# Optimization experiments

Hardware: AMD Instinct MI355X
Metric: run time of the kernel (lower is better)

Reference implementation:

```python
import jax, jax.numpy as jnp
import numpy as np

HIDDEN = 2048
N_HEADS = 16
N_KV = 2
HEAD_DIM = HIDDEN // N_HEADS  # 128


def setup_inputs() -> dict:
    key = jax.random.key(0)
    ks = jax.random.split(key, 9)
    s = 0.02
    kv_dim = N_KV * HEAD_DIM
    return {
        "hidden_states": jax.random.normal(ks[0], (2, 2048, HIDDEN), jnp.float32),
        "Wq": jax.random.normal(ks[1], (HIDDEN, HIDDEN), jnp.float32) * s,
        "bq": jnp.zeros((HIDDEN,), jnp.float32),
        "Wk": jax.random.normal(ks[2], (HIDDEN, kv_dim), jnp.float32) * s,
        "bk": jnp.zeros((kv_dim,), jnp.float32),
        "Wv": jax.random.normal(ks[3], (HIDDEN, kv_dim), jnp.float32) * s,
        "bv": jnp.zeros((kv_dim,), jnp.float32),
        "Wo": jax.random.normal(ks[4], (HIDDEN, HIDDEN), jnp.float32) * s,
        "bo": jnp.zeros((HIDDEN,), jnp.float32),
    }


def reference(hidden_states, Wq, bq, Wk, bk, Wv, bv, Wo, bo):
    B, S, _ = hidden_states.shape
    scaling = HEAD_DIM ** (-0.5)
    rep = N_HEADS // N_KV

    q = hidden_states @ Wq + bq                      # [B,S,H*D]
    k = hidden_states @ Wk + bk                      # [B,S,KV*D]
    v = hidden_states @ Wv + bv

    q = q.reshape(B, S, N_HEADS, HEAD_DIM) * scaling
    k = k.reshape(B, S, N_KV, HEAD_DIM)
    v = v.reshape(B, S, N_KV, HEAD_DIM)
    # repeat_interleave KV heads to match query heads (faithful to source)
    k = jnp.repeat(k, rep, axis=2)                   # [B,S,H,D]
    v = jnp.repeat(v, rep, axis=2)

    attn = jnp.einsum('bqhd,bkhd->bhqk', q, k)       # [B,H,S,S] score matrix
    attn = jax.nn.softmax(attn, axis=-1)
    out = jnp.einsum('bhqk,bkhd->bqhd', attn, v)     # [B,S,H,D]
    out = out.reshape(B, S, N_HEADS * HEAD_DIM)
    return out @ Wo + bo
```

## Files before the change

kernel.cpp:

```cpp
#include <hip/hip_runtime.h>

typedef __bf16 bf16;
typedef __bf16 bf16x4 __attribute__((ext_vector_type(4)));
typedef __bf16 bf16x8 __attribute__((ext_vector_type(8)));
typedef float  f32x4  __attribute__((ext_vector_type(4)));

#define AS1 __attribute__((address_space(1)))
#define AS3 __attribute__((address_space(3)))

__device__ __forceinline__ void gload_lds16(const void* g, void* l) {
    __builtin_amdgcn_global_load_lds((const AS1 void*)g, (AS3 void*)l, 16, 0, 0);
}

__global__ __launch_bounds__(256) void prep(
    const float* __restrict__ X,  const float* __restrict__ Wq,
    const float* __restrict__ Wk, const float* __restrict__ Wv,
    const float* __restrict__ Wo, const float* __restrict__ bq,
    const float* __restrict__ bk, const float* __restrict__ bv,
    bf16* __restrict__ Xb, bf16* __restrict__ Wqkvt,
    bf16* __restrict__ Wot, float* __restrict__ bqkv)
{
    __shared__ float tile[32][33];
    int bid = blockIdx.x;
    if (bid < 8192) {
        int i = bid * 256 + threadIdx.x;
        float4 v = ((const float4*)X)[i];
        bf16x4 o = { (bf16)v.x, (bf16)v.y, (bf16)v.z, (bf16)v.w };
        ((bf16x4*)Xb)[i] = o;
        return;
    }
    bid -= 8192;
    const float* src; bf16* dst; int R, C, bx, by;
    if (bid < 4096)      { src = Wq; dst = Wqkvt;                      R = 2048; C = 2048; bx = bid & 63; by = bid >> 6; }
    else if (bid < 4608) { int t = bid - 4096; src = Wk; dst = Wqkvt + (size_t)2048 * 2048; R = 2048; C = 256; bx = t & 7; by = t >> 3; }
    else if (bid < 5120) { int t = bid - 4608; src = Wv; dst = Wqkvt + (size_t)2304 * 2048; R = 2048; C = 256; bx = t & 7; by = t >> 3; }
    else if (bid < 9216) { int t = bid - 5120; src = Wo; dst = Wot;    R = 2048; C = 2048; bx = t & 63; by = t >> 6; }
    else {
        int i = (bid - 9216) * 256 + threadIdx.x;
        if (i < 2048) bqkv[i] = bq[i];
        else if (i < 2304) bqkv[i] = bk[i - 2048];
        else if (i < 2560) bqkv[i] = bv[i - 2304];
        return;
    }
    int tx = threadIdx.x & 31, tg = threadIdx.x >> 5;
    int c0 = bx * 32, r0 = by * 32;
    #pragma unroll
    for (int j = tg; j < 32; j += 8)
        tile[j][tx] = src[(size_t)(r0 + j) * C + c0 + tx];
    __syncthreads();
    #pragma unroll
    for (int j = tg; j < 32; j += 8)
        dst[(size_t)(c0 + j) * R + r0 + tx] = (bf16)tile[tx][j];
}

__global__ __launch_bounds__(256) void transpose_v(
    const bf16* __restrict__ KV, bf16* __restrict__ VT)
{
    const int t = threadIdx.x;
    const int dg = t & 15;
    const int cg = (blockIdx.x << 4) | (t >> 4);
    const int kvh = blockIdx.y, b = blockIdx.z;
    const int tile = cg >> 3, cl = cg & 7;
    const int k0 = ((cl & 4) << 3) | ((cl & 3) << 2);

    const bf16* src = KV + ((size_t)(b * 2048 + tile * 64 + k0) * 512) + 256 + kvh * 128 + dg * 8;
    bf16x8 col[8];
    #pragma unroll
    for (int e = 0; e < 8; ++e) {
        int koff = ((e & 4) << 2) | (e & 3);
        col[e] = *(const bf16x8*)(src + (size_t)koff * 512);
    }
    bf16* dst = VT + ((size_t)((b * 2 + kvh) * 128 + dg * 8)) * 2048 + cg * 8;
    #pragma unroll
    for (int j = 0; j < 8; ++j) {
        bf16x8 row;
        #pragma unroll
        for (int e = 0; e < 8; ++e) row[e] = col[e][j];
        *(bf16x8*)(dst + (size_t)j * 2048) = row;
    }
}

template<int OUTBF>
__global__ __launch_bounds__(256) void gemm_bt(
    const bf16* __restrict__ A, const bf16* __restrict__ Bt,
    const float* __restrict__ bias, void* __restrict__ Cv,
    int M, int N, int K, float scale)
{
    __shared__ bf16 As[128 * 32];
    __shared__ bf16 Bs[128 * 32];
    const int tid = threadIdx.x;
    const int l = tid & 63, w = tid >> 6;
    const int wm = w >> 1, wn = w & 1;
    const size_t rowBase = (size_t)blockIdx.y * 128;
    const size_t colBase = (size_t)blockIdx.x * 128;

    f32x4 acc[4][4] = {};

    const int srow = l >> 2;
    const int schunk = (l & 3) ^ ((l >> 3) & 3);
    const int frow = l & 15;
    const int fswz = (frow >> 1) & 3;
    const int g = l >> 4;

    const bf16* Ag = A  + (rowBase + w * 32 + srow) * (size_t)K + schunk * 8;
    const bf16* Bg = Bt + (colBase + w * 32 + srow) * (size_t)K + schunk * 8;

    for (int k0 = 0; k0 < K; k0 += 32) {
        gload_lds16(Ag + k0,                  As + (w * 32) * 32);
        gload_lds16(Ag + 16 * (size_t)K + k0, As + (w * 32 + 16) * 32);
        gload_lds16(Bg + k0,                  Bs + (w * 32) * 32);
        gload_lds16(Bg + 16 * (size_t)K + k0, Bs + (w * 32 + 16) * 32);
        __syncthreads();

        bf16x8 af[4], bfr[4];
        #pragma unroll
        for (int mi = 0; mi < 4; ++mi)
            af[mi] = *(const bf16x8*)(As + (wm * 64 + mi * 16 + frow) * 32 + ((g ^ fswz) << 3));
        #pragma unroll
        for (int ni = 0; ni < 4; ++ni)
            bfr[ni] = *(const bf16x8*)(Bs + (wn * 64 + ni * 16 + frow) * 32 + ((g ^ fswz) << 3));
        #pragma unroll
        for (int mi = 0; mi < 4; ++mi)
            #pragma unroll
            for (int ni = 0; ni < 4; ++ni)
                acc[mi][ni] = __builtin_amdgcn_mfma_f32_16x16x32_bf16(af[mi], bfr[ni], acc[mi][ni], 0, 0, 0);
        __syncthreads();
    }

    const int cr = (l >> 4) * 4;
    const int cc = l & 15;
    #pragma unroll
    for (int ni = 0; ni < 4; ++ni) {
        const int col = (int)colBase + wn * 64 + ni * 16 + cc;
        const float bv = bias[col];
        #pragma unroll
        for (int mi = 0; mi < 4; ++mi) {
            #pragma unroll
            for (int r = 0; r < 4; ++r) {
                const size_t row = rowBase + wm * 64 + mi * 16 + cr + r;
                float v = (acc[mi][ni][r] + bv) * scale;
                if (OUTBF) ((bf16*)Cv)[row * N + col] = (bf16)v;
                else       ((float*)Cv)[row * N + col] = v;
            }
        }
    }
}

__global__ __launch_bounds__(256) void gemm_qkv(
    const bf16* __restrict__ A, const bf16* __restrict__ Bt,
    const float* __restrict__ bias, bf16* __restrict__ Qb, bf16* __restrict__ KVb,
    float qscale)
{
    constexpr int K = 2048;
    __shared__ bf16 As[128 * 32];
    __shared__ bf16 Bs[128 * 32];
    const int tid = threadIdx.x;
    const int l = tid & 63, w = tid >> 6;
    const int wm = w >> 1, wn = w & 1;
    const size_t rowBase = (size_t)blockIdx.y * 128;
    const size_t colBase = (size_t)blockIdx.x * 128;

    f32x4 acc[4][4] = {};

    const int srow = l >> 2;
    const int schunk = (l & 3) ^ ((l >> 3) & 3);
    const int frow = l & 15;
    const int fswz = (frow >> 1) & 3;
    const int g = l >> 4;

    const bf16* Ag = A  + (rowBase + w * 32 + srow) * (size_t)K + schunk * 8;
    const bf16* Bg = Bt + (colBase + w * 32 + srow) * (size_t)K + schunk * 8;

    for (int k0 = 0; k0 < K; k0 += 32) {
        gload_lds16(Ag + k0,                  As + (w * 32) * 32);
        gload_lds16(Ag + 16 * (size_t)K + k0, As + (w * 32 + 16) * 32);
        gload_lds16(Bg + k0,                  Bs + (w * 32) * 32);
        gload_lds16(Bg + 16 * (size_t)K + k0, Bs + (w * 32 + 16) * 32);
        __syncthreads();

        bf16x8 af[4], bfr[4];
        #pragma unroll
        for (int mi = 0; mi < 4; ++mi)
            af[mi] = *(const bf16x8*)(As + (wm * 64 + mi * 16 + frow) * 32 + ((g ^ fswz) << 3));
        #pragma unroll
        for (int ni = 0; ni < 4; ++ni)
            bfr[ni] = *(const bf16x8*)(Bs + (wn * 64 + ni * 16 + frow) * 32 + ((g ^ fswz) << 3));
        #pragma unroll
        for (int mi = 0; mi < 4; ++mi)
            #pragma unroll
            for (int ni = 0; ni < 4; ++ni)
                acc[mi][ni] = __builtin_amdgcn_mfma_f32_16x16x32_bf16(af[mi], bfr[ni], acc[mi][ni], 0, 0, 0);
        __syncthreads();
    }

    const bool isQ = colBase < 2048;
    bf16* Cb = isQ ? Qb : KVb;
    const int ldc = isQ ? 2048 : 512;
    const int coff = isQ ? 0 : 2048;
    const float s = isQ ? qscale : 1.0f;

    const int cr = (l >> 4) * 4;
    const int cc = l & 15;
    #pragma unroll
    for (int ni = 0; ni < 4; ++ni) {
        const int col = (int)colBase + wn * 64 + ni * 16 + cc;
        const float bv = bias[col];
        #pragma unroll
        for (int mi = 0; mi < 4; ++mi) {
            #pragma unroll
            for (int r = 0; r < 4; ++r) {
                const size_t row = rowBase + wm * 64 + mi * 16 + cr + r;
                Cb[row * ldc + (col - coff)] = (bf16)((acc[mi][ni][r] + bv) * s);
            }
        }
    }
}

__global__ __launch_bounds__(512, 4) void attn_fwd(
    const bf16* __restrict__ Q, const bf16* __restrict__ KV,
    const bf16* __restrict__ VT, bf16* __restrict__ O)
{
    constexpr int S = 2048;
    constexpr int LDKV = 512;
    constexpr int NT = S / 64;
    __shared__ bf16 Ks[2][64 * 128];
    __shared__ bf16 VTs[2][128 * 64];

    const int tid = threadIdx.x;
    const int l = tid & 63, w = tid >> 6;
    const int qt = blockIdx.x, h = blockIdx.y, b = blockIdx.z;
    const int kvh = h >> 3;
    const int lg = l >> 4, ll = l & 15;
    const int eh = (ll >> 2) & 1;

    bf16x8 qf[4];
    {
        const bf16* qp = Q + ((size_t)(b * S + qt * 128 + w * 16 + ll)) * 2048 + h * 128 + lg * 8;
        #pragma unroll
        for (int j = 0; j < 4; ++j) qf[j] = *(const bf16x8*)(qp + (j << 5));
    }

    const bf16* Kg  = KV + (size_t)b * S * LDKV + kvh * 128;
    const bf16* VTg = VT + ((size_t)(b * 2 + kvh) * 128) * S;

    const bf16* kg0 = Kg + (size_t)(w * 8 + lg) * LDKV + (ll ^ lg) * 8;
    const bf16* kg1 = Kg + (size_t)(w * 8 + 4 + lg) * LDKV + (ll ^ (4 + lg)) * 8;
    const bf16* vg0 = VTg + (size_t)(w * 16 + (l >> 3)) * S + (((l & 7) ^ ((l >> 3) & 7)) << 3);
    const bf16* vg1 = vg0 + 8 * (size_t)S;
    const int kd0 = (w * 8) * 128;
    const int kd1 = (w * 8 + 4) * 128;
    const int vd0 = w * 1024;
    const int vd1 = w * 1024 + 512;

    const int swz8 = (lg ^ (ll & 3)) << 3;
    const int kbE = ll * 128 + swz8 + eh * 32;
    const int kbO = ll * 128 + swz8 + (1 - eh) * 32;
    const int vbE = ll * 64 + swz8 + eh * 32;
    const int vbO = ll * 64 + swz8 + (1 - eh) * 32;

    bf16x8 vones;
    #pragma unroll
    for (int e = 0; e < 8; ++e) vones[e] = (bf16)1.0f;

    f32x4 of[8] = {};
    f32x4 of_l = {};

    gload_lds16(kg0, &Ks[0][kd0]);
    gload_lds16(kg1, &Ks[0][kd1]);
    gload_lds16(vg0, &VTs[0][vd0]);
    gload_lds16(vg1, &VTs[0][vd1]);
    __syncthreads();

    for (int t = 0; t < NT; ++t) {
        const int buf = t & 1;
        const bf16* kE = &Ks[buf][kbE];
        const bf16* kO = &Ks[buf][kbO];
        const bf16* vE = &VTs[buf][vbE];
        const bf16* vO = &VTs[buf][vbO];

        if (t + 1 < NT) {
            const size_t ko = (size_t)(t + 1) * 64 * LDKV;
            const int    vo = (t + 1) * 64;
            gload_lds16(kg0 + ko, &Ks[buf ^ 1][kd0]);
            gload_lds16(kg1 + ko, &Ks[buf ^ 1][kd1]);
            gload_lds16(vg0 + vo, &VTs[buf ^ 1][vd0]);
            gload_lds16(vg1 + vo, &VTs[buf ^ 1][vd1]);
        }

        f32x4 sc[4] = {};
        __builtin_amdgcn_s_setprio(1);
        #pragma unroll
        for (int ni = 0; ni < 4; ++ni) {
            bf16x8 k0f = *(const bf16x8*)(kE + ni * 2048);
            sc[ni] = __builtin_amdgcn_mfma_f32_16x16x32_bf16(k0f, qf[0], sc[ni], 0, 0, 0);
            bf16x8 k1f = *(const bf16x8*)(kO + ni * 2048);
            sc[ni] = __builtin_amdgcn_mfma_f32_16x16x32_bf16(k1f, qf[1], sc[ni], 0, 0, 0);
            bf16x8 k2f = *(const bf16x8*)(kE + ni * 2048 + 64);
            sc[ni] = __builtin_amdgcn_mfma_f32_16x16x32_bf16(k2f, qf[2], sc[ni], 0, 0, 0);
            bf16x8 k3f = *(const bf16x8*)(kO + ni * 2048 + 64);
            sc[ni] = __builtin_amdgcn_mfma_f32_16x16x32_bf16(k3f, qf[3], sc[ni], 0, 0, 0);
        }
        __builtin_amdgcn_s_setprio(0);

        float p[4][4];
        #pragma unroll
        for (int ni = 0; ni < 4; ++ni)
            #pragma unroll
            for (int r = 0; r < 4; ++r)
                p[ni][r] = __builtin_exp2f(sc[ni][r]);

        bf16x8 pa0, pa1;
        #pragma unroll
        for (int e = 0; e < 8; ++e) {
            pa0[e] = (bf16)p[(e >> 2)][e & 3];
            pa1[e] = (bf16)p[2 + (e >> 2)][e & 3];
        }

        __builtin_amdgcn_s_setprio(1);
        of_l = __builtin_amdgcn_mfma_f32_16x16x32_bf16(pa0, vones, of_l, 0, 0, 0);
        #pragma unroll
        for (int nf = 0; nf < 8; ++nf) {
            bf16x8 v0 = *(const bf16x8*)(vE + nf * 1024);
            of[nf] = __builtin_amdgcn_mfma_f32_16x16x32_bf16(pa0, v0, of[nf], 0, 0, 0);
        }
        of_l = __builtin_amdgcn_mfma_f32_16x16x32_bf16(pa1, vones, of_l, 0, 0, 0);
        #pragma unroll
        for (int nf = 0; nf < 8; ++nf) {
            bf16x8 v1 = *(const bf16x8*)(vO + nf * 1024);
            of[nf] = __builtin_amdgcn_mfma_f32_16x16x32_bf16(pa1, v1, of[nf], 0, 0, 0);
        }
        __builtin_amdgcn_s_setprio(0);

        __syncthreads();
    }

    #pragma unroll
    for (int r = 0; r < 4; ++r) {
        float inv = 1.0f / of_l[r];
        size_t row = (size_t)(b * S + qt * 128 + w * 16 + lg * 4 + r);
        bf16* op = O + row * 2048 + h * 128 + ll;
        #pragma unroll
        for (int nf = 0; nf < 8; ++nf)
            op[nf * 16] = (bf16)(of[nf][r] * inv);
    }
}

extern "C" void kernel_launch(void* const* d_in, const int* in_sizes, int n_in,
                              void* d_out, int out_size, void* d_ws, size_t ws_size,
                              hipStream_t stream)
{
    const float* X  = (const float*)d_in[0];
    const float* Wq = (const float*)d_in[1];
    const float* bq = (const float*)d_in[2];
    const float* Wk = (const float*)d_in[3];
    const float* bk = (const float*)d_in[4];
    const float* Wv = (const float*)d_in[5];
    const float* bv = (const float*)d_in[6];
    const float* Wo = (const float*)d_in[7];
    const float* bo = (const float*)d_in[8];
    float* out = (float*)d_out;

    bf16* p = (bf16*)d_ws;
    bf16* Xb    = p; p += 8388608;
    bf16* Qb    = p; p += 8388608;
    bf16* KVbuf = p; p += 2097152;
    bf16* VTb   = p; p += 1048576;
    bf16* Wqkvt = p; p += 5242880;
    bf16* Wot   = p; p += 4194304;
    float* bqkv = (float*)p; p += 5120;
    bf16* Oattn = Xb;

    const float qscale = 0.12751744f;

    prep<<<17418, 256, 0, stream>>>(X, Wq, Wk, Wv, Wo, bq, bk, bv,
                                    Xb, Wqkvt, Wot, bqkv);

    gemm_qkv<<<dim3(20, 32), 256, 0, stream>>>(Xb, Wqkvt, bqkv, Qb, KVbuf, qscale);

    transpose_v<<<dim3(16, 2, 2), 256, 0, stream>>>(KVbuf, VTb);

    attn_fwd<<<dim3(16, 16, 2), 512, 0, stream>>>(Qb, KVbuf, VTb, Oattn);

    gemm_bt<0><<<dim3(16, 32), 256, 0, stream>>>(Oattn, Wot, bo, out, 4096, 2048, 2048, 1.0f);
}
```

Baseline: 236.7 us.

## Fuse V transpose into QKV GEMM epilogue and software-pipeline PV in attention

The QKV GEMM epilogue now writes K to its own buffer and writes V directly in the transposed, permuted layout, so the separate transpose_v kernel and its launch go away. The attention kernel triple-buffers V in dynamic shared memory and defers each tile's P·V MFMAs to the next iteration, letting them overlap the next QK^T and exp computation. The cost is a larger LDS footprint (80KB), which may lower occupancy, plus scattered 8-byte V stores in the GEMM epilogue.

```diff
diff --git a/kernel.cpp b/kernel.cpp
--- a/kernel.cpp
+++ b/kernel.cpp
@@ -53,33 +53,6 @@
         dst[(size_t)(c0 + j) * R + r0 + tx] = (bf16)tile[tx][j];
 }
 
-__global__ __launch_bounds__(256) void transpose_v(
-    const bf16* __restrict__ KV, bf16* __restrict__ VT)
-{
-    const int t = threadIdx.x;
-    const int dg = t & 15;
-    const int cg = (blockIdx.x << 4) | (t >> 4);
-    const int kvh = blockIdx.y, b = blockIdx.z;
-    const int tile = cg >> 3, cl = cg & 7;
-    const int k0 = ((cl & 4) << 3) | ((cl & 3) << 2);
-
-    const bf16* src = KV + ((size_t)(b * 2048 + tile * 64 + k0) * 512) + 256 + kvh * 128 + dg * 8;
-    bf16x8 col[8];
-    #pragma unroll
-    for (int e = 0; e < 8; ++e) {
-        int koff = ((e & 4) << 2) | (e & 3);
-        col[e] = *(const bf16x8*)(src + (size_t)koff * 512);
-    }
-    bf16* dst = VT + ((size_t)((b * 2 + kvh) * 128 + dg * 8)) * 2048 + cg * 8;
-    #pragma unroll
-    for (int j = 0; j < 8; ++j) {
-        bf16x8 row;
-        #pragma unroll
-        for (int e = 0; e < 8; ++e) row[e] = col[e][j];
-        *(bf16x8*)(dst + (size_t)j * 2048) = row;
-    }
-}
-
 template<int OUTBF>
 __global__ __launch_bounds__(256) void gemm_bt(
     const bf16* __restrict__ A, const bf16* __restrict__ Bt,
@@ -148,8 +121,8 @@
 
 __global__ __launch_bounds__(256) void gemm_qkv(
     const bf16* __restrict__ A, const bf16* __restrict__ Bt,
-    const float* __restrict__ bias, bf16* __restrict__ Qb, bf16* __restrict__ KVb,
-    float qscale)
+    const float* __restrict__ bias, bf16* __restrict__ Qb, bf16* __restrict__ Kb,
+    bf16* __restrict__ VT, float qscale)
 {
     constexpr int K = 2048;
     __shared__ bf16 As[128 * 32];
@@ -193,38 +166,56 @@
         __syncthreads();
     }
 
-    const bool isQ = colBase < 2048;
-    bf16* Cb = isQ ? Qb : KVb;
-    const int ldc = isQ ? 2048 : 512;
-    const int coff = isQ ? 0 : 2048;
-    const float s = isQ ? qscale : 1.0f;
-
     const int cr = (l >> 4) * 4;
     const int cc = l & 15;
+    const int cb = (int)colBase;
     #pragma unroll
     for (int ni = 0; ni < 4; ++ni) {
-        const int col = (int)colBase + wn * 64 + ni * 16 + cc;
+        const int col = cb + wn * 64 + ni * 16 + cc;
         const float bv = bias[col];
-        #pragma unroll
-        for (int mi = 0; mi < 4; ++mi) {
-            #pragma unroll
-            for (int r = 0; r < 4; ++r) {
-                const size_t row = rowBase + wm * 64 + mi * 16 + cr + r;
-                Cb[row * ldc + (col - coff)] = (bf16)((acc[mi][ni][r] + bv) * s);
+        if (cb < 2048) {
+            #pragma unroll
+            for (int mi = 0; mi < 4; ++mi)
+                #pragma unroll
+                for (int r = 0; r < 4; ++r) {
+                    const size_t row = rowBase + wm * 64 + mi * 16 + cr + r;
+                    Qb[row * 2048 + col] = (bf16)((acc[mi][ni][r] + bv) * qscale);
+                }
+        } else if (cb < 2304) {
+            #pragma unroll
+            for (int mi = 0; mi < 4; ++mi)
+                #pragma unroll
+                for (int r = 0; r < 4; ++r) {
+                    const size_t row = rowBase + wm * 64 + mi * 16 + cr + r;
+                    Kb[row * 256 + (col - 2048)] = (bf16)(acc[mi][ni][r] + bv);
+                }
+        } else {
+            const int vcol = col - 2304;
+            const int kvh = vcol >> 7, d = vcol & 127;
+            #pragma unroll
+            for (int mi = 0; mi < 4; ++mi) {
+                const size_t row0 = rowBase + wm * 64 + mi * 16 + cr;
+                const int bb = (int)(row0 >> 11);
+                const int s  = (int)(row0 & 2047);
+                const int tile = s >> 6, sp = s & 63;
+                const int slot = (sp & 35) | ((sp & 8) << 1) | ((sp & 4) << 1) | ((sp & 16) >> 2);
+                bf16x4 v4 = { (bf16)(acc[mi][ni][0] + bv), (bf16)(acc[mi][ni][1] + bv),
+                              (bf16)(acc[mi][ni][2] + bv), (bf16)(acc[mi][ni][3] + bv) };
+                *(bf16x4*)(VT + ((size_t)((bb * 2 + kvh) * 128 + d)) * 2048 + tile * 64 + slot) = v4;
             }
         }
     }
 }
 
 __global__ __launch_bounds__(512, 4) void attn_fwd(
-    const bf16* __restrict__ Q, const bf16* __restrict__ KV,
+    const bf16* __restrict__ Q, const bf16* __restrict__ Kb,
     const bf16* __restrict__ VT, bf16* __restrict__ O)
 {
     constexpr int S = 2048;
-    constexpr int LDKV = 512;
     constexpr int NT = S / 64;
-    __shared__ bf16 Ks[2][64 * 128];
-    __shared__ bf16 VTs[2][128 * 64];
+    extern __shared__ bf16 smem[];
+    bf16* Ks = smem;
+    bf16* Vs = smem + 16384;
 
     const int tid = threadIdx.x;
     const int l = tid & 63, w = tid >> 6;
@@ -240,11 +231,11 @@
         for (int j = 0; j < 4; ++j) qf[j] = *(const bf16x8*)(qp + (j << 5));
     }
 
-    const bf16* Kg  = KV + (size_t)b * S * LDKV + kvh * 128;
+    const bf16* Kg  = Kb + (size_t)b * S * 256 + kvh * 128;
     const bf16* VTg = VT + ((size_t)(b * 2 + kvh) * 128) * S;
 
-    const bf16* kg0 = Kg + (size_t)(w * 8 + lg) * LDKV + (ll ^ lg) * 8;
-    const bf16* kg1 = Kg + (size_t)(w * 8 + 4 + lg) * LDKV + (ll ^ (4 + lg)) * 8;
+    const bf16* kg0 = Kg + (size_t)(w * 8 + lg) * 256 + (ll ^ lg) * 8;
+    const bf16* kg1 = Kg + (size_t)(w * 8 + 4 + lg) * 256 + (ll ^ (4 + lg)) * 8;
     const bf16* vg0 = VTg + (size_t)(w * 16 + (l >> 3)) * S + (((l & 7) ^ ((l >> 3) & 7)) << 3);
     const bf16* vg1 = vg0 + 8 * (size_t)S;
     const int kd0 = (w * 8) * 128;
@@ -264,29 +255,28 @@
 
     f32x4 of[8] = {};
     f32x4 of_l = {};
-
-    gload_lds16(kg0, &Ks[0][kd0]);
-    gload_lds16(kg1, &Ks[0][kd1]);
-    gload_lds16(vg0, &VTs[0][vd0]);
-    gload_lds16(vg1, &VTs[0][vd1]);
+    bf16x8 paA, paB;
+
+    gload_lds16(kg0, Ks + kd0);
+    gload_lds16(kg1, Ks + kd1);
+    gload_lds16(vg0, Vs + vd0);
+    gload_lds16(vg1, Vs + vd1);
     __syncthreads();
 
+    int sP = 2, sC = 0, sN = 1;
     for (int t = 0; t < NT; ++t) {
         const int buf = t & 1;
-        const bf16* kE = &Ks[buf][kbE];
-        const bf16* kO = &Ks[buf][kbO];
-        const bf16* vE = &VTs[buf][vbE];
-        const bf16* vO = &VTs[buf][vbO];
-
         if (t + 1 < NT) {
-            const size_t ko = (size_t)(t + 1) * 64 * LDKV;
+            const size_t ko = (size_t)(t + 1) * 64 * 256;
             const int    vo = (t + 1) * 64;
-            gload_lds16(kg0 + ko, &Ks[buf ^ 1][kd0]);
-            gload_lds16(kg1 + ko, &Ks[buf ^ 1][kd1]);
-            gload_lds16(vg0 + vo, &VTs[buf ^ 1][vd0]);
-            gload_lds16(vg1 + vo, &VTs[buf ^ 1][vd1]);
-        }
-
+            gload_lds16(kg0 + ko, Ks + (buf ^ 1) * 8192 + kd0);
+            gload_lds16(kg1 + ko, Ks + (buf ^ 1) * 8192 + kd1);
+            gload_lds16(vg0 + vo, Vs + sN * 8192 + vd0);
+            gload_lds16(vg1 + vo, Vs + sN * 8192 + vd1);
+        }
+
+        const bf16* kE = Ks + buf * 8192 + kbE;
+        const bf16* kO = Ks + buf * 8192 + kbO;
         f32x4 sc[4] = {};
         __builtin_amdgcn_s_setprio(1);
         #pragma unroll
@@ -302,36 +292,58 @@
         }
         __builtin_amdgcn_s_setprio(0);
 
+        if (t > 0) {
+            const bf16* vE = Vs + sP * 8192 + vbE;
+            const bf16* vO = Vs + sP * 8192 + vbO;
+            __builtin_amdgcn_s_setprio(1);
+            of_l = __builtin_amdgcn_mfma_f32_16x16x32_bf16(paA, vones, of_l, 0, 0, 0);
+            #pragma unroll
+            for (int nf = 0; nf < 8; ++nf) {
+                bf16x8 v0 = *(const bf16x8*)(vE + nf * 1024);
+                of[nf] = __builtin_amdgcn_mfma_f32_16x16x32_bf16(paA, v0, of[nf], 0, 0, 0);
+            }
+            of_l = __builtin_amdgcn_mfma_f32_16x16x32_bf16(paB, vones, of_l, 0, 0, 0);
+            #pragma unroll
+            for (int nf = 0; nf < 8; ++nf) {
+                bf16x8 v1 = *(const bf16x8*)(vO + nf * 1024);
+                of[nf] = __builtin_amdgcn_mfma_f32_16x16x32_bf16(paB, v1, of[nf], 0, 0, 0);
+            }
+            __builtin_amdgcn_s_setprio(0);
+        }
+
         float p[4][4];
         #pragma unroll
         for (int ni = 0; ni < 4; ++ni)
             #pragma unroll
             for (int r = 0; r < 4; ++r)
                 p[ni][r] = __builtin_exp2f(sc[ni][r]);
-
-        bf16x8 pa0, pa1;
+        bf16x8 npa0, npa1;
         #pragma unroll
         for (int e = 0; e < 8; ++e) {
-            pa0[e] = (bf16)p[(e >> 2)][e & 3];
-            pa1[e] = (bf16)p[2 + (e >> 2)][e & 3];
-        }
-
-        __builtin_amdgcn_s_setprio(1);
-        of_l = __builtin_amdgcn_mfma_f32_16x16x32_bf16(pa0, vones, of_l, 0, 0, 0);
+            npa0[e] = (bf16)p[(e >> 2)][e & 3];
+            npa1[e] = (bf16)p[2 + (e >> 2)][e & 3];
+        }
+        paA = npa0; paB = npa1;
+
+        __syncthreads();
+        int tmp = sP; sP = sC; sC = sN; sN = tmp;
+    }
+
+    {
+        const bf16* vE = Vs + sP * 8192 + vbE;
+        const bf16* vO = Vs + sP * 8192 + vbO;
+        of_l = __builtin_amdgcn_mfma_f32_16x16x32_bf16(paA, vones, of_l, 0, 0, 0);
         #pragma unroll
         for (int nf = 0; nf < 8; ++nf) {
             bf16x8 v0 = *(const bf16x8*)(vE + nf * 1024);
-            of[nf] = __builtin_amdgcn_mfma_f32_16x16x32_bf16(pa0, v0, of[nf], 0, 0, 0);
-        }
-        of_l = __builtin_amdgcn_mfma_f32_16x16x32_bf16(pa1, vones, of_l, 0, 0, 0);
+            of[nf] = __builtin_amdgcn_mfma_f32_16x16x32_bf16(paA, v0, of[nf], 0, 0, 0);
+        }
+        of_l = __builtin_amdgcn_mfma_f32_16x16x32_bf16(paB, vones, of_l, 0, 0, 0);
         #pragma unroll
         for (int nf = 0; nf < 8; ++nf) {
             bf16x8 v1 = *(const bf16x8*)(vO + nf * 1024);
-            of[nf] = __builtin_amdgcn_mfma_f32_16x16x32_bf16(pa1, v1, of[nf], 0, 0, 0);
-        }
-        __builtin_amdgcn_s_setprio(0);
-
-        __syncthreads();
+            of[nf] = __builtin_amdgcn_mfma_f32_16x16x32_bf16(paB, v1, of[nf], 0, 0, 0);
+        }
     }
 
     #pragma unroll
@@ -363,7 +375,7 @@
     bf16* p = (bf16*)d_ws;
     bf16* Xb    = p; p += 8388608;
     bf16* Qb    = p; p += 8388608;
-    bf16* KVbuf = p; p += 2097152;
+    bf16* Kbuf  = p; p += 1048576;
     bf16* VTb   = p; p += 1048576;
     bf16* Wqkvt = p; p += 5242880;
     bf16* Wot   = p; p += 4194304;
@@ -372,14 +384,15 @@
 
     const float qscale = 0.12751744f;
 
+    (void)hipFuncSetAttribute((const void*)attn_fwd,
+                              hipFuncAttributeMaxDynamicSharedMemorySize, 81920);
+
     prep<<<17418, 256, 0, stream>>>(X, Wq, Wk, Wv, Wo, bq, bk, bv,
                                     Xb, Wqkvt, Wot, bqkv);
 
-    gemm_qkv<<<dim3(20, 32), 256, 0, stream>>>(Xb, Wqkvt, bqkv, Qb, KVbuf, qscale);
-
-    transpose_v<<<dim3(16, 2, 2), 256, 0, stream>>>(KVbuf, VTb);
-
-    attn_fwd<<<dim3(16, 16, 2), 512, 0, stream>>>(Qb, KVbuf, VTb, Oattn);
+    gemm_qkv<<<dim3(20, 32), 256, 0, stream>>>(Xb, Wqkvt, bqkv, Qb, Kbuf, VTb, qscale);
+
+    attn_fwd<<<dim3(16, 16, 2), 512, 81920, stream>>>(Qb, Kbuf, VTb, Oattn);
 
     gemm_bt<0><<<dim3(16, 32), 256, 0, stream>>>(Oattn, Wot, bo, out, 4096, 2048, 2048, 1.0f);
 }
```

Measured after the change: 202.9 us. 14.3% less time.
